# Kernel optimization log

Measured on AMD Instinct MI355X. Metric: run time of the kernel, lower is better.

## Reference

```python
import jax, jax.numpy as jnp
import numpy as np

B, S, IN_DIM, OUT_DIM = 4, 2048, 1024, 1024
NEG = -9e15

def _xavier(key, shape, gain=1.414):
    fan_in, fan_out = shape[0], shape[1]
    a = gain * np.sqrt(6.0 / (fan_in + fan_out))
    return jax.random.uniform(key, shape, jnp.float32, -a, a)

def setup_inputs() -> dict:
    key = jax.random.key(0)
    ks = jax.random.split(key, 8)
    x = jax.random.normal(ks[0], (B, S, IN_DIM), jnp.float32)
    W_query = _xavier(ks[1], (IN_DIM, OUT_DIM))
    W_key = _xavier(ks[2], (IN_DIM, OUT_DIM))
    W_value = _xavier(ks[3], (IN_DIM, OUT_DIM))
    # torch Linear default init (kaiming-uniform-ish); values don't matter for correctness baseline
    W1 = _xavier(ks[4], (OUT_DIM + IN_DIM, OUT_DIM), gain=1.0)
    b1 = jnp.zeros((OUT_DIM,), jnp.float32)
    W2 = _xavier(ks[5], (OUT_DIM, OUT_DIM), gain=1.0)
    b2 = jnp.zeros((OUT_DIM,), jnp.float32)
    return {"x": x, "W_query": W_query, "W_key": W_key, "W_value": W_value,
            "W1": W1, "b1": b1, "W2": W2, "b2": b2}

def reference(x, W_query, W_key, W_value, W1, b1, W2, b2):
    # QKV projections: [B,S,in] @ [in,out] -> [B,S,out]
    q = jnp.einsum('bsi,io->bso', x, W_query)
    k = jnp.einsum('bsi,io->bso', x, W_key)
    v = jnp.einsum('bsi,io->bso', x, W_value)
    scale = 1.0 / jnp.sqrt(jnp.float32(OUT_DIM))
    e = jnp.einsum('bqd,bkd->bqk', q, k) * scale  # [B,S,S]
    causal = jnp.tril(jnp.ones((S, S), jnp.float32))  # mask > 0 keeps lower triangle
    attn = jnp.where(causal > 0, e, jnp.float32(NEG))
    attn = jax.nn.softmax(attn, axis=2)
    # dropout: eval mode (train=False) -> identity
    out = jnp.einsum('bqk,bkd->bqd', attn, v)  # [B,S,out]
    h = jnp.concatenate([out, x], axis=-1)  # [B,S,out+in]
    h = jax.nn.relu(jnp.einsum('bsf,fo->bso', h, W1) + b1)
    return jnp.einsum('bsf,fo->bso', h, W2) + b2
```

## Files before the change

kernel.cpp:

```cpp
#include <hip/hip_runtime.h>
#include <stdint.h>

typedef __attribute__((ext_vector_type(8))) short short8;
typedef __attribute__((ext_vector_type(4))) short short4v;
typedef __attribute__((ext_vector_type(4))) float f32x4;

__device__ __forceinline__ unsigned short f32_to_bf16(float f) {
    unsigned int u = __float_as_uint(f);
    u += 0x7FFFu + ((u >> 16) & 1u);
    return (unsigned short)(u >> 16);
}

__device__ __forceinline__ short8 load8_f32_as_bf16(const float* __restrict__ ap) {
    f32x4 f0 = *(const f32x4*)ap;
    f32x4 f1 = *(const f32x4*)(ap + 4);
    union { short8 s; unsigned short u[8]; } cv;
#pragma unroll
    for (int t = 0; t < 4; ++t) {
        cv.u[t]     = f32_to_bf16(f0[t]);
        cv.u[t + 4] = f32_to_bf16(f1[t]);
    }
    return cv.s;
}

__device__ __forceinline__ void gld_lds16(const void* g, void* l) {
    __builtin_amdgcn_global_load_lds(
        (const __attribute__((address_space(1))) unsigned int*)(unsigned long long)(uintptr_t)g,
        (__attribute__((address_space(3))) unsigned int*)(unsigned int)(uintptr_t)l,
        16, 0, 0);
}

template<int MT>
__global__ __launch_bounds__(256, 4)
void gemm128(const unsigned short* __restrict__ A,
             int lda,
             const unsigned short* __restrict__ B, int ldb,
             void* __restrict__ C, int ldc, int K,
             long bStride, long cStride,
             void* __restrict__ C2, int ldc2)
{
    int z = blockIdx.z;
    int mblk, nblk;
    {
        int x = blockIdx.x, yy = blockIdx.y;
        if (z < 2) { mblk = x * 8 + (yy & 7); nblk = yy >> 3; }
        else       { nblk = x * 8 + (yy & 7); mblk = yy >> 3; }
    }
    int m0 = mblk * MT;
    int n0 = nblk * 128;

    const unsigned short* Ab;
    const unsigned short* Bb;
    if (z < 2) { Ab = A; Bb = B + (size_t)z * bStride; }
    else       { Ab = B + (size_t)2 * bStride; Bb = A; }

    __shared__ __align__(16) short As[MT * 64];
    __shared__ __align__(16) short Bs[128 * 64];

    int tid  = threadIdx.x;
    int lane = tid & 63, wid = tid >> 6;
    constexpr int MI = MT / 32;
    int wm = (wid & 1) * (MT / 2), wn = (wid >> 1) * 64;
    int fr = lane & 15, fq = lane >> 4;
    int sw0 = ((fq    ) ^ (fr & 7)) * 16;
    int sw1 = ((fq ^ 4) ^ (fr & 7)) * 16;

    int rS = tid >> 3;
    int cS = ((tid & 7) ^ (rS & 7)) * 8;
    char* AsB = (char*)As; char* BsB = (char*)Bs;

    f32x4 acc[MI][4];
#pragma unroll
    for (int i = 0; i < MI; ++i)
#pragma unroll
    for (int j = 0; j < 4; ++j) acc[i][j] = f32x4{0.f, 0.f, 0.f, 0.f};

    for (int k0 = 0; k0 < K; k0 += 64) {
        const unsigned short* pa = Ab + (size_t)(m0 + rS) * lda + k0 + cS;
        const unsigned short* pb = Bb + (size_t)(n0 + rS) * ldb + k0 + cS;
#pragma unroll
        for (int t = 0; t < MT / 32; ++t)
            gld_lds16(pa + (size_t)(32 * t) * lda, AsB + t * 4096 + tid * 16);
#pragma unroll
        for (int t = 0; t < 4; ++t)
            gld_lds16(pb + (size_t)(32 * t) * ldb,  BsB + t * 4096 + tid * 16);
        __syncthreads();

#pragma unroll
        for (int kh = 0; kh < 2; ++kh) {
            int sw = kh ? sw1 : sw0;
            short8 a[MI], b[4];
#pragma unroll
            for (int i = 0; i < MI; ++i)
                a[i] = *(const short8*)(AsB + (wm + i * 16 + fr) * 128 + sw);
#pragma unroll
            for (int j = 0; j < 4; ++j)
                b[j] = *(const short8*)(BsB + (wn + j * 16 + fr) * 128 + sw);
#pragma unroll
            for (int i = 0; i < MI; ++i)
#pragma unroll
            for (int j = 0; j < 4; ++j)
                acc[i][j] = __builtin_amdgcn_mfma_f32_16x16x32_bf16(a[i], b[j], acc[i][j], 0, 0, 0);
        }
        __syncthreads();
    }

    unsigned short* Cz; int ldcz;
    if (z >= 2) { Cz = (unsigned short*)C2; ldcz = ldc2; }
    else { Cz = (unsigned short*)C + (size_t)z * cStride; ldcz = ldc; }
#pragma unroll
    for (int i = 0; i < MI; ++i)
#pragma unroll
    for (int j = 0; j < 4; ++j)
#pragma unroll
    for (int r = 0; r < 4; ++r) {
        int row = m0 + wm + i * 16 + fq * 4 + r;
        int col = n0 + wn + j * 16 + fr;
        Cz[(size_t)row * ldcz + col] = f32_to_bf16(acc[i][j][r]);
    }
}

template<int EPI, int SWIZ, bool KLIMIT>
__global__ __launch_bounds__(256, 2)
void gemmdb(const unsigned short* __restrict__ A,
            int lda,
            const unsigned short* __restrict__ B, int ldb,
            void* __restrict__ C, int ldc, int K,
            long aStride, long bStride, long cStride,
            const float* __restrict__ bias, long biasStride, float scale)
{
    int z = blockIdx.z;
    int mblk, nblk;
    if (SWIZ == 5) {
        int x = blockIdx.x;
        int per = (int)gridDim.x >> 3;
        x = (x & 7) * per + (x >> 3);
        int a = (int)sqrtf(2.f * (float)x + 1.f);
        if (a > 15) a = 15;
        while (a < 15 && ((a + 1) * (a + 2) / 2) <= x) ++a;
        while (a > 0 && (a * (a + 1) / 2) > x) --a;
        mblk = a;
        nblk = x - a * (a + 1) / 2;
    } else if (SWIZ == 7) {
        int glin = (int)blockIdx.z * 128 + (int)blockIdx.y * 8 + (int)blockIdx.x;
        int xcd = glin & 7;
        int s   = glin >> 3;
        z = xcd >> 1;
        int h  = xcd & 1;
        int jm = s & 7;
        nblk   = s >> 3;
        mblk   = (jm & 1) ? (15 - h - (jm >> 1) * 2) : ((jm >> 1) * 2 + h);
    } else {
        mblk = blockIdx.y;
        nblk = blockIdx.x;
    }
    int m0 = mblk * 128;
    int n0 = nblk * 128;

    const unsigned short* Ab = A + (size_t)z * aStride;
    const unsigned short* Bb = B + (size_t)z * bStride;

    __shared__ __align__(16) char lds[65536];

    int tid  = threadIdx.x;
    int lane = tid & 63, wid = tid >> 6;
    int wm = (wid & 1) * 64, wn = (wid >> 1) * 64;
    int fr = lane & 15, fq = lane >> 4;
    int sw0 = ((fq    ) ^ (fr & 7)) * 16;
    int sw1 = ((fq ^ 4) ^ (fr & 7)) * 16;

    int rS = tid >> 3;
    int cS = ((tid & 7) ^ (rS & 7)) * 8;

    int kend = KLIMIT ? min(K, m0 + 128) : K;
    int NT = kend >> 6;

    f32x4 acc[4][4];
#pragma unroll
    for (int i = 0; i < 4; ++i)
#pragma unroll
    for (int j = 0; j < 4; ++j) acc[i][j] = f32x4{0.f, 0.f, 0.f, 0.f};

    auto STAGE = [&](int kt) {
        char* dst = lds + (kt & 1) * 32768;
        const unsigned short* pa = Ab + (size_t)(m0 + rS) * lda + (kt << 6) + cS;
        const unsigned short* pb = Bb + (size_t)(n0 + rS) * ldb + (kt << 6) + cS;
#pragma unroll
        for (int u = 0; u < 4; ++u)
            gld_lds16(pa + (size_t)(32 * u) * lda, dst + u * 4096 + tid * 16);
#pragma unroll
        for (int u = 0; u < 4; ++u)
            gld_lds16(pb + (size_t)(32 * u) * ldb, dst + 16384 + u * 4096 + tid * 16);
    };

    STAGE(0);
    for (int t = 0; t < NT; ++t) {
        if (t + 1 < NT) {
            STAGE(t + 1);
            asm volatile("s_waitcnt vmcnt(8)" ::: "memory");
        } else {
            asm volatile("s_waitcnt vmcnt(0)" ::: "memory");
        }
        __builtin_amdgcn_s_barrier();
        __builtin_amdgcn_sched_barrier(0);
        const char* AsB = (const char*)lds + (t & 1) * 32768;
        const char* BsB = AsB + 16384;
#pragma unroll
        for (int kh = 0; kh < 2; ++kh) {
            int sw = kh ? sw1 : sw0;
            short8 a[4], b[4];
#pragma unroll
            for (int i = 0; i < 4; ++i)
                a[i] = *(const short8*)(AsB + (wm + i * 16 + fr) * 128 + sw);
#pragma unroll
            for (int j = 0; j < 4; ++j)
                b[j] = *(const short8*)(BsB + (wn + j * 16 + fr) * 128 + sw);
            __builtin_amdgcn_s_setprio(1);
#pragma unroll
            for (int i = 0; i < 4; ++i)
#pragma unroll
            for (int j = 0; j < 4; ++j)
                acc[i][j] = __builtin_amdgcn_mfma_f32_16x16x32_bf16(a[i], b[j], acc[i][j], 0, 0, 0);
            __builtin_amdgcn_s_setprio(0);
        }
        __builtin_amdgcn_s_barrier();
        __builtin_amdgcn_sched_barrier(0);
        asm volatile("" ::: "memory");
    }

    if (EPI == 6) {
        unsigned short* Cz = (unsigned short*)C + (size_t)z * cStride;
        float* rs = const_cast<float*>(bias) + z * biasStride;
#pragma unroll
        for (int i = 0; i < 4; ++i)
#pragma unroll
        for (int r = 0; r < 4; ++r) {
            int row = m0 + wm + i * 16 + fq * 4 + r;
            float s = 0.f;
#pragma unroll
            for (int j = 0; j < 4; ++j) {
                int col = n0 + wn + j * 16 + fr;
                float e = (col <= row) ? __expf(acc[i][j][r] * scale - 16.f) : 0.f;
                s += e;
                Cz[(size_t)row * ldc + col] = f32_to_bf16(e);
            }
            s += __shfl_xor(s, 1);
            s += __shfl_xor(s, 2);
            s += __shfl_xor(s, 4);
            s += __shfl_xor(s, 8);
            if (fr == 0) atomicAdd(&rs[row], s);
        }
    } else {
        unsigned short* Cz = (unsigned short*)C + (size_t)z * cStride;
#pragma unroll
        for (int i = 0; i < 4; ++i)
#pragma unroll
        for (int r = 0; r < 4; ++r) {
            int row = m0 + wm + i * 16 + fq * 4 + r;
            float inv = 1.f / bias[z * biasStride + row];
#pragma unroll
            for (int j = 0; j < 4; ++j) {
                int col = n0 + wn + j * 16 + fr;
                Cz[(size_t)row * ldc + col] = f32_to_bf16(acc[i][j][r] * inv);
            }
        }
    }
}

template<int AMODE, int EPI>
__global__ __launch_bounds__(512, 2)
void gemm8p(const unsigned short* __restrict__ A, const unsigned short* __restrict__ A2,
            int lda, int lda2, int ksplit,
            const unsigned short* __restrict__ B, int ldb,
            void* __restrict__ C, int ldc, int K,
            const float* __restrict__ bias)
{
    int lin = blockIdx.y * gridDim.x + blockIdx.x;
    int xcd = lin & 7, idx = lin >> 3;
    int mch = (int)gridDim.y >> 3;
    int mblk = xcd * mch + idx % mch;
    int nblk = idx / mch;
    int m0 = mblk * 256, n0 = nblk * 128;

    constexpr int TILE = 49152;
    __shared__ __align__(16) char lds[3 * TILE];

    int tid  = threadIdx.x;
    int lane = tid & 63, wid = tid >> 6;
    int wm = (wid & 3) * 64, wn = (wid >> 2) * 64;
    int fr = lane & 15, fq = lane >> 4;
    int sw0 = ((fq    ) ^ (fr & 7)) * 16;
    int sw1 = ((fq ^ 4) ^ (fr & 7)) * 16;

    int rS = tid >> 3;
    int cS = ((tid & 7) ^ (rS & 7)) * 8;

    int NT = K >> 6;

    f32x4 acc[4][4];
#pragma unroll
    for (int i = 0; i < 4; ++i)
#pragma unroll
    for (int j = 0; j < 4; ++j) acc[i][j] = f32x4{0.f, 0.f, 0.f, 0.f};

    auto STAGE = [&](int t, int slot) {
        int k0 = t << 6;
        char* dst = lds + slot * TILE;
        const unsigned short* Asrc = A; int koff = k0, ldax = lda;
        if (AMODE == 2 && k0 >= ksplit) { Asrc = A2; koff = k0 - ksplit; ldax = lda2; }
        const unsigned short* pa = Asrc + (size_t)(m0 + rS) * ldax + koff + cS;
        const unsigned short* pb = B    + (size_t)(n0 + rS) * ldb  + k0   + cS;
#pragma unroll
        for (int u = 0; u < 4; ++u)
            gld_lds16(pa + (size_t)(64 * u) * ldax, dst + u * 8192 + tid * 16);
#pragma unroll
        for (int u = 0; u < 2; ++u)
            gld_lds16(pb + (size_t)(64 * u) * ldb, dst + 32768 + u * 8192 + tid * 16);
    };

    STAGE(0, 0);
    STAGE(1, 1);
    asm volatile("s_waitcnt vmcnt(6)" ::: "memory");
    __builtin_amdgcn_s_barrier();
    __builtin_amdgcn_sched_barrier(0);
    asm volatile("" ::: "memory");

    int sc = 0, ss = 2;
    for (int t = 0; t < NT; ++t) {
        if (t + 2 < NT) STAGE(t + 2, ss);
        const char* AsB = (const char*)(lds + sc * TILE);
        const char* BsB = AsB + 32768;
#pragma unroll
        for (int kh = 0; kh < 2; ++kh) {
            int sw = kh ? sw1 : sw0;
            short8 a[4], b[4];
#pragma unroll
            for (int i = 0; i < 4; ++i)
                a[i] = *(const short8*)(AsB + (wm + i * 16 + fr) * 128 + sw);
#pragma unroll
            for (int j = 0; j < 4; ++j)
                b[j] = *(const short8*)(BsB + (wn + j * 16 + fr) * 128 + sw);
            __builtin_amdgcn_s_setprio(1);
#pragma unroll
            for (int i = 0; i < 4; ++i)
#pragma unroll
            for (int j = 0; j < 4; ++j)
                acc[i][j] = __builtin_amdgcn_mfma_f32_16x16x32_bf16(a[i], b[j], acc[i][j], 0, 0, 0);
            __builtin_amdgcn_s_setprio(0);
        }
        if (t + 1 < NT) {
            if (t + 2 < NT) { asm volatile("s_waitcnt vmcnt(6)" ::: "memory"); }
            else            { asm volatile("s_waitcnt vmcnt(0)" ::: "memory"); }
            __builtin_amdgcn_s_barrier();
            __builtin_amdgcn_sched_barrier(0);
            asm volatile("" ::: "memory");
        }
        sc = sc == 2 ? 0 : sc + 1;
        ss = ss == 2 ? 0 : ss + 1;
    }

#pragma unroll
    for (int i = 0; i < 4; ++i)
#pragma unroll
    for (int j = 0; j < 4; ++j)
#pragma unroll
    for (int r = 0; r < 4; ++r) {
        int row = m0 + wm + i * 16 + fq * 4 + r;
        int col = n0 + wn + j * 16 + fr;
        float v = acc[i][j][r];
        if (EPI == 2) {
            v += bias[col];
            v = v > 0.f ? v : 0.f;
            ((unsigned short*)C)[(size_t)row * ldc + col] = f32_to_bf16(v);
        } else {
            ((float*)C)[(size_t)row * ldc + col] = v + bias[col];
        }
    }
}

__device__ __forceinline__ void transpose_tile64(const float* __restrict__ in,
                                                 unsigned short* __restrict__ out,
                                                 int rows, int cols, int bx, int by, int tid)
{
    __shared__ float t[64][65];
    int tx = tid & 15, ty = tid >> 4;
    int r0 = by * 64, c0 = bx * 64;
#pragma unroll
    for (int i = 0; i < 4; ++i) {
        f32x4 v = *(const f32x4*)(in + (size_t)(r0 + ty + i * 16) * cols + c0 + tx * 4);
#pragma unroll
        for (int j = 0; j < 4; ++j) t[ty + i * 16][tx * 4 + j] = v[j];
    }
    __syncthreads();
#pragma unroll
    for (int i = 0; i < 4; ++i) {
        union { short4v s; unsigned short u[4]; } o;
#pragma unroll
        for (int j = 0; j < 4; ++j) o.u[j] = f32_to_bf16(t[tx * 4 + j][ty + i * 16]);
        *(short4v*)(out + (size_t)(c0 + ty + i * 16) * rows + r0 + tx * 4) = o.s;
    }
}

__global__ __launch_bounds__(256)
void prep_kernel(const float* __restrict__ x,
                 const float* __restrict__ Wq, const float* __restrict__ Wk,
                 const float* __restrict__ Wv, const float* __restrict__ W1,
                 const float* __restrict__ W2,
                 unsigned short* __restrict__ xb, unsigned short* __restrict__ WT,
                 unsigned short* __restrict__ W1T, unsigned short* __restrict__ W2T,
                 float* __restrict__ rsum)
{
    int idx = blockIdx.x;
    int tid = threadIdx.x;
    if (idx < 1024) {
#pragma unroll
        for (int it = 0; it < 4; ++it) {
            size_t i = ((size_t)idx * 4 + it) * 2048 + (size_t)tid * 8;
            *(short8*)(xb + i) = load8_f32_as_bf16(x + i);
        }
    } else if (idx < 1792) {
        int t = idx - 1024;
        int w = t >> 8; t &= 255;
        const float* in = w == 0 ? Wq : (w == 1 ? Wk : Wv);
        transpose_tile64(in, WT + (size_t)w * 1024 * 1024, 1024, 1024,
                         t & 15, t >> 4, tid);
    } else if (idx < 2304) {
        int t = idx - 1792;
        transpose_tile64(W1, W1T, 2048, 1024, t & 15, t >> 4, tid);
    } else if (idx < 2560) {
        int t = idx - 2304;
        transpose_tile64(W2, W2T, 1024, 1024, t & 15, t >> 4, tid);
    } else {
        int t = idx - 2560;
        f32x4 zero = {0.f, 0.f, 0.f, 0.f};
        float* p = rsum + ((size_t)t * 256 + tid) * 8;
        *(f32x4*)p = zero;
        *(f32x4*)(p + 4) = zero;
    }
}

extern "C" void kernel_launch(void* const* d_in, const int* in_sizes, int n_in,
                              void* d_out, int out_size, void* d_ws, size_t ws_size,
                              hipStream_t stream)
{
    const float* x  = (const float*)d_in[0];
    const float* Wq = (const float*)d_in[1];
    const float* Wk = (const float*)d_in[2];
    const float* Wv = (const float*)d_in[3];
    const float* W1 = (const float*)d_in[4];
    const float* b1 = (const float*)d_in[5];
    const float* W2 = (const float*)d_in[6];
    const float* b2 = (const float*)d_in[7];
    float* out = (float*)d_out;

    size_t off = 0;
    auto alloc = [&](size_t bytes) {
        char* r = (char*)d_ws + off;
        off += (bytes + 255) & ~(size_t)255;
        return r;
    };
    const size_t TOK = (size_t)8192 * 1024;
    unsigned short* WT   = (unsigned short*)alloc((size_t)3072 * 1024 * 2);
    unsigned short* W1T  = (unsigned short*)alloc((size_t)1024 * 2048 * 2);
    unsigned short* W2T  = (unsigned short*)alloc((size_t)1024 * 1024 * 2);
    unsigned short* xb   = (unsigned short*)alloc(TOK * 2);
    unsigned short* vT   = (unsigned short*)alloc((size_t)1024 * 8192 * 2);
    unsigned short* attn = (unsigned short*)alloc(TOK * 2);
    float*          rsum = (float*)         alloc((size_t)4 * 2048 * 4);
    unsigned short* q    = (unsigned short*)alloc(TOK * 2);
    unsigned short* k    = (unsigned short*)alloc(TOK * 2);
    unsigned short* S    = (unsigned short*)alloc((size_t)4 * 2048 * 2048 * 2);
    unsigned short* h1   = S;

    prep_kernel<<<2564, 256, 0, stream>>>(x, Wq, Wk, Wv, W1, W2, xb, WT, W1T, W2T, rsum);

    gemm128<128><<<dim3(8, 64, 3), 256, 0, stream>>>(
        xb, 1024, WT, 1024, q, 1024, 1024,
        (long)1024 * 1024, (long)TOK, vT, 8192);

    gemmdb<6, 5, false><<<dim3(136, 1, 4), 256, 0, stream>>>(
        q, 1024, k, 1024, S, 2048, 1024,
        (long)2048 * 1024, (long)2048 * 1024, (long)2048 * 2048, rsum, 2048, 0.03125f);

    gemmdb<4, 7, true><<<dim3(8, 16, 4), 256, 0, stream>>>(
        S, 2048, vT, 8192, attn, 1024, 2048,
        (long)2048 * 2048, (long)2048, (long)2048 * 1024, rsum, 2048, 0.f);

    gemm8p<2, 2><<<dim3(8, 32, 1), 512, 0, stream>>>(
        attn, xb, 1024, 1024, 1024, W1T, 2048, h1, 1024, 2048, b1);

    gemm8p<0, 3><<<dim3(8, 32, 1), 512, 0, stream>>>(
        h1, nullptr, 1024, 0, 0, W2T, 1024, out, 1024, 1024, b2);
}
```

Measured before the change: 285.4 us.

## Compute V-transpose projection concurrently with causal score GEMM in one launch

The V projection (vT = WvT·xb^T) moves out of the QKV projection launch and into a combined kernel that also computes the causal QK^T scores with the exp/rowsum epilogue. Blocks 0-543 handle triangular score tiles and blocks 544+ handle V tiles, so the two independent GEMMs share one grid and fill the GPU better than the 544-block triangular launch alone. The merged kernel uses a single-buffered 128x128 tile loop at 4 blocks/CU instead of gemmdb's double-buffered schedule for the scores, which may lower per-tile efficiency on the score part.

```diff
diff --git a/kernel.cpp b/kernel.cpp
--- a/kernel.cpp
+++ b/kernel.cpp
@@ -36,23 +36,16 @@
              int lda,
              const unsigned short* __restrict__ B, int ldb,
              void* __restrict__ C, int ldc, int K,
-             long bStride, long cStride,
-             void* __restrict__ C2, int ldc2)
+             long bStride, long cStride)
 {
     int z = blockIdx.z;
-    int mblk, nblk;
-    {
-        int x = blockIdx.x, yy = blockIdx.y;
-        if (z < 2) { mblk = x * 8 + (yy & 7); nblk = yy >> 3; }
-        else       { nblk = x * 8 + (yy & 7); mblk = yy >> 3; }
-    }
+    int mblk = blockIdx.x * 8 + (blockIdx.y & 7);
+    int nblk = blockIdx.y >> 3;
     int m0 = mblk * MT;
     int n0 = nblk * 128;
 
-    const unsigned short* Ab;
-    const unsigned short* Bb;
-    if (z < 2) { Ab = A; Bb = B + (size_t)z * bStride; }
-    else       { Ab = B + (size_t)2 * bStride; Bb = A; }
+    const unsigned short* Ab = A;
+    const unsigned short* Bb = B + (size_t)z * bStride;
 
     __shared__ __align__(16) short As[MT * 64];
     __shared__ __align__(16) short Bs[128 * 64];
@@ -105,9 +98,7 @@
         __syncthreads();
     }
 
-    unsigned short* Cz; int ldcz;
-    if (z >= 2) { Cz = (unsigned short*)C2; ldcz = ldc2; }
-    else { Cz = (unsigned short*)C + (size_t)z * cStride; ldcz = ldc; }
+    unsigned short* Cz = (unsigned short*)C + (size_t)z * cStride;
 #pragma unroll
     for (int i = 0; i < MI; ++i)
 #pragma unroll
@@ -116,44 +107,148 @@
     for (int r = 0; r < 4; ++r) {
         int row = m0 + wm + i * 16 + fq * 4 + r;
         int col = n0 + wn + j * 16 + fr;
-        Cz[(size_t)row * ldcz + col] = f32_to_bf16(acc[i][j][r]);
-    }
-}
-
-template<int EPI, int SWIZ, bool KLIMIT>
+        Cz[(size_t)row * ldc + col] = f32_to_bf16(acc[i][j][r]);
+    }
+}
+
+__global__ __launch_bounds__(256, 4)
+void scorevt(const unsigned short* __restrict__ q,
+             const unsigned short* __restrict__ k,
+             unsigned short* __restrict__ S, float* __restrict__ rsum,
+             float scale,
+             const unsigned short* __restrict__ WvT,
+             const unsigned short* __restrict__ xb,
+             unsigned short* __restrict__ vT)
+{
+    int glin = blockIdx.x;
+    bool isV = glin >= 544;
+    int z = 0, m0, n0;
+    const unsigned short *Ab, *Bb;
+    if (!isV) {
+        int t = (glin & 7) * 68 + (glin >> 3);
+        z = t / 136;
+        int tri = t - z * 136;
+        int a = (int)sqrtf(2.f * (float)tri + 1.f);
+        if (a > 15) a = 15;
+        while (a < 15 && ((a + 1) * (a + 2) / 2) <= tri) ++a;
+        while (a > 0 && (a * (a + 1) / 2) > tri) --a;
+        m0 = a * 128;
+        n0 = (tri - a * (a + 1) / 2) * 128;
+        Ab = q + (size_t)z * 2048 * 1024;
+        Bb = k + (size_t)z * 2048 * 1024;
+    } else {
+        int g2 = glin - 544;
+        int xcd = g2 & 7, idx = g2 >> 3;
+        int nblk = xcd * 8 + (idx & 7);
+        int mblk = idx >> 3;
+        m0 = mblk * 128;
+        n0 = nblk * 128;
+        Ab = WvT;
+        Bb = xb;
+    }
+
+    __shared__ __align__(16) short As[128 * 64];
+    __shared__ __align__(16) short Bs[128 * 64];
+
+    int tid  = threadIdx.x;
+    int lane = tid & 63, wid = tid >> 6;
+    int wm = (wid & 1) * 64, wn = (wid >> 1) * 64;
+    int fr = lane & 15, fq = lane >> 4;
+    int sw0 = ((fq    ) ^ (fr & 7)) * 16;
+    int sw1 = ((fq ^ 4) ^ (fr & 7)) * 16;
+
+    int rS = tid >> 3;
+    int cS = ((tid & 7) ^ (rS & 7)) * 8;
+    char* AsB = (char*)As; char* BsB = (char*)Bs;
+
+    f32x4 acc[4][4];
+#pragma unroll
+    for (int i = 0; i < 4; ++i)
+#pragma unroll
+    for (int j = 0; j < 4; ++j) acc[i][j] = f32x4{0.f, 0.f, 0.f, 0.f};
+
+    for (int k0 = 0; k0 < 1024; k0 += 64) {
+        const unsigned short* pa = Ab + (size_t)(m0 + rS) * 1024 + k0 + cS;
+        const unsigned short* pb = Bb + (size_t)(n0 + rS) * 1024 + k0 + cS;
+#pragma unroll
+        for (int t = 0; t < 4; ++t)
+            gld_lds16(pa + (size_t)(32 * t) * 1024, AsB + t * 4096 + tid * 16);
+#pragma unroll
+        for (int t = 0; t < 4; ++t)
+            gld_lds16(pb + (size_t)(32 * t) * 1024, BsB + t * 4096 + tid * 16);
+        __syncthreads();
+
+#pragma unroll
+        for (int kh = 0; kh < 2; ++kh) {
+            int sw = kh ? sw1 : sw0;
+            short8 a[4], b[4];
+#pragma unroll
+            for (int i = 0; i < 4; ++i)
+                a[i] = *(const short8*)(AsB + (wm + i * 16 + fr) * 128 + sw);
+#pragma unroll
+            for (int j = 0; j < 4; ++j)
+                b[j] = *(const short8*)(BsB + (wn + j * 16 + fr) * 128 + sw);
+#pragma unroll
+            for (int i = 0; i < 4; ++i)
+#pragma unroll
+            for (int j = 0; j < 4; ++j)
+                acc[i][j] = __builtin_amdgcn_mfma_f32_16x16x32_bf16(a[i], b[j], acc[i][j], 0, 0, 0);
+        }
+        __syncthreads();
+    }
+
+    if (!isV) {
+        unsigned short* Cz = S + (size_t)z * 2048 * 2048;
+        float* rs = rsum + (size_t)z * 2048;
+#pragma unroll
+        for (int i = 0; i < 4; ++i)
+#pragma unroll
+        for (int r = 0; r < 4; ++r) {
+            int row = m0 + wm + i * 16 + fq * 4 + r;
+            float s = 0.f;
+#pragma unroll
+            for (int j = 0; j < 4; ++j) {
+                int col = n0 + wn + j * 16 + fr;
+                float e = (col <= row) ? __expf(acc[i][j][r] * scale - 16.f) : 0.f;
+                s += e;
+                Cz[(size_t)row * 2048 + col] = f32_to_bf16(e);
+            }
+            s += __shfl_xor(s, 1);
+            s += __shfl_xor(s, 2);
+            s += __shfl_xor(s, 4);
+            s += __shfl_xor(s, 8);
+            if (fr == 0) atomicAdd(&rs[row], s);
+        }
+    } else {
+#pragma unroll
+        for (int i = 0; i < 4; ++i)
+#pragma unroll
+        for (int j = 0; j < 4; ++j)
+#pragma unroll
+        for (int r = 0; r < 4; ++r) {
+            int row = m0 + wm + i * 16 + fq * 4 + r;
+            int col = n0 + wn + j * 16 + fr;
+            vT[(size_t)row * 8192 + col] = f32_to_bf16(acc[i][j][r]);
+        }
+    }
+}
+
 __global__ __launch_bounds__(256, 2)
 void gemmdb(const unsigned short* __restrict__ A,
             int lda,
             const unsigned short* __restrict__ B, int ldb,
             void* __restrict__ C, int ldc, int K,
             long aStride, long bStride, long cStride,
-            const float* __restrict__ bias, long biasStride, float scale)
-{
-    int z = blockIdx.z;
-    int mblk, nblk;
-    if (SWIZ == 5) {
-        int x = blockIdx.x;
-        int per = (int)gridDim.x >> 3;
-        x = (x & 7) * per + (x >> 3);
-        int a = (int)sqrtf(2.f * (float)x + 1.f);
-        if (a > 15) a = 15;
-        while (a < 15 && ((a + 1) * (a + 2) / 2) <= x) ++a;
-        while (a > 0 && (a * (a + 1) / 2) > x) --a;
-        mblk = a;
-        nblk = x - a * (a + 1) / 2;
-    } else if (SWIZ == 7) {
-        int glin = (int)blockIdx.z * 128 + (int)blockIdx.y * 8 + (int)blockIdx.x;
-        int xcd = glin & 7;
-        int s   = glin >> 3;
-        z = xcd >> 1;
-        int h  = xcd & 1;
-        int jm = s & 7;
-        nblk   = s >> 3;
-        mblk   = (jm & 1) ? (15 - h - (jm >> 1) * 2) : ((jm >> 1) * 2 + h);
-    } else {
-        mblk = blockIdx.y;
-        nblk = blockIdx.x;
-    }
+            const float* __restrict__ bias, long biasStride)
+{
+    int glin = (int)blockIdx.z * 128 + (int)blockIdx.y * 8 + (int)blockIdx.x;
+    int xcd = glin & 7;
+    int s   = glin >> 3;
+    int z = xcd >> 1;
+    int h  = xcd & 1;
+    int jm = s & 7;
+    int nblk = s >> 3;
+    int mblk = (jm & 1) ? (15 - h - (jm >> 1) * 2) : ((jm >> 1) * 2 + h);
     int m0 = mblk * 128;
     int n0 = nblk * 128;
 
@@ -172,7 +267,7 @@
     int rS = tid >> 3;
     int cS = ((tid & 7) ^ (rS & 7)) * 8;
 
-    int kend = KLIMIT ? min(K, m0 + 128) : K;
+    int kend = min(K, m0 + 128);
     int NT = kend >> 6;
 
     f32x4 acc[4][4];
@@ -228,41 +323,17 @@
         asm volatile("" ::: "memory");
     }
 
-    if (EPI == 6) {
-        unsigned short* Cz = (unsigned short*)C + (size_t)z * cStride;
-        float* rs = const_cast<float*>(bias) + z * biasStride;
-#pragma unroll
-        for (int i = 0; i < 4; ++i)
-#pragma unroll
-        for (int r = 0; r < 4; ++r) {
-            int row = m0 + wm + i * 16 + fq * 4 + r;
-            float s = 0.f;
-#pragma unroll
-            for (int j = 0; j < 4; ++j) {
-                int col = n0 + wn + j * 16 + fr;
-                float e = (col <= row) ? __expf(acc[i][j][r] * scale - 16.f) : 0.f;
-                s += e;
-                Cz[(size_t)row * ldc + col] = f32_to_bf16(e);
-            }
-            s += __shfl_xor(s, 1);
-            s += __shfl_xor(s, 2);
-            s += __shfl_xor(s, 4);
-            s += __shfl_xor(s, 8);
-            if (fr == 0) atomicAdd(&rs[row], s);
-        }
-    } else {
-        unsigned short* Cz = (unsigned short*)C + (size_t)z * cStride;
-#pragma unroll
-        for (int i = 0; i < 4; ++i)
-#pragma unroll
-        for (int r = 0; r < 4; ++r) {
-            int row = m0 + wm + i * 16 + fq * 4 + r;
-            float inv = 1.f / bias[z * biasStride + row];
-#pragma unroll
-            for (int j = 0; j < 4; ++j) {
-                int col = n0 + wn + j * 16 + fr;
-                Cz[(size_t)row * ldc + col] = f32_to_bf16(acc[i][j][r] * inv);
-            }
+    unsigned short* Cz = (unsigned short*)C + (size_t)z * cStride;
+#pragma unroll
+    for (int i = 0; i < 4; ++i)
+#pragma unroll
+    for (int r = 0; r < 4; ++r) {
+        int row = m0 + wm + i * 16 + fq * 4 + r;
+        float inv = 1.f / bias[z * biasStride + row];
+#pragma unroll
+        for (int j = 0; j < 4; ++j) {
+            int col = n0 + wn + j * 16 + fr;
+            Cz[(size_t)row * ldc + col] = f32_to_bf16(acc[i][j][r] * inv);
         }
     }
 }
@@ -474,17 +545,16 @@
 
     prep_kernel<<<2564, 256, 0, stream>>>(x, Wq, Wk, Wv, W1, W2, xb, WT, W1T, W2T, rsum);
 
-    gemm128<128><<<dim3(8, 64, 3), 256, 0, stream>>>(
+    gemm128<128><<<dim3(8, 64, 2), 256, 0, stream>>>(
         xb, 1024, WT, 1024, q, 1024, 1024,
-        (long)1024 * 1024, (long)TOK, vT, 8192);
-
-    gemmdb<6, 5, false><<<dim3(136, 1, 4), 256, 0, stream>>>(
-        q, 1024, k, 1024, S, 2048, 1024,
-        (long)2048 * 1024, (long)2048 * 1024, (long)2048 * 2048, rsum, 2048, 0.03125f);
-
-    gemmdb<4, 7, true><<<dim3(8, 16, 4), 256, 0, stream>>>(
+        (long)1024 * 1024, (long)TOK);
+
+    scorevt<<<1056, 256, 0, stream>>>(
+        q, k, S, rsum, 0.03125f, WT + (size_t)2 * 1024 * 1024, xb, vT);
+
+    gemmdb<<<dim3(8, 16, 4), 256, 0, stream>>>(
         S, 2048, vT, 8192, attn, 1024, 2048,
-        (long)2048 * 2048, (long)2048, (long)2048 * 1024, rsum, 2048, 0.f);
+        (long)2048 * 2048, (long)2048, (long)2048 * 1024, rsum, 2048);
 
     gemm8p<2, 2><<<dim3(8, 32, 1), 512, 0, stream>>>(
         attn, xb, 1024, 1024, 1024, W1T, 2048, h1, 1024, 2048, b1);
```

Result: faster. 277.6 us (median of 2 runs) (-2.7%).
